# Kernel optimization log

Hardware: AMD Instinct MI355X
Metric: run time of the kernel (lower is better)

Reference implementation:

```python
import jax, jax.numpy as jnp
import numpy as np

N = 100000   # nodes
E = 3200000  # edges
F_IN = 64    # input feature dim
H = 64       # hidden dim
G = 512      # graphs in batch
C = 6        # classes
BN_EPS = 1e-5


def setup_inputs() -> dict:
    key = jax.random.key(0)
    ks = jax.random.split(key, 24)

    def nrm(i, shape, s=0.05):
        return jax.random.normal(ks[i], shape, jnp.float32) * s

    d = {}
    d["x"] = jax.random.normal(ks[0], (N, F_IN), jnp.float32)
    d["edge_index"] = jax.random.randint(ks[1], (2, E), 0, N, dtype=jnp.int32)
    d["batch"] = jnp.sort(jax.random.randint(ks[2], (N,), 0, G, dtype=jnp.int32))
    # GIN MLP weights (conv4 reuses conv3's MLP, matching the original code)
    for li, fin in [(1, F_IN), (2, H), (3, H)]:
        d[f"w{li}a"] = nrm(2 + li * 4, (fin, H))
        d[f"b{li}a"] = jnp.zeros((H,), jnp.float32)
        d[f"w{li}b"] = nrm(3 + li * 4, (H, H))
        d[f"b{li}b"] = jnp.zeros((H,), jnp.float32)
    # learnable eps (train_eps=True, init 0) and BN affine params per layer
    for li in range(1, 5):
        d[f"eps{li}"] = jnp.float32(0.0)
        d[f"g{li}"] = jnp.ones((H,), jnp.float32)
        d[f"be{li}"] = jnp.zeros((H,), jnp.float32)
    d["wfc"] = nrm(20, (2 * H, C))
    d["bfc"] = jnp.zeros((C,), jnp.float32)
    return d


def gin_block(x, src, dst, eps, wa, ba, wb, bb, gamma, beta):
    # neighbor sum aggregation: messages flow src -> dst
    agg = jax.ops.segment_sum(x[src], dst, num_segments=N)
    h = (1.0 + eps) * x + agg
    h = jax.nn.relu(h @ wa + ba) @ wb + bb  # GIN MLP
    h = jax.nn.relu(h)
    # BatchNorm1d over the node dimension (training-mode batch stats)
    mu = h.mean(axis=0)
    var = h.var(axis=0)
    return (h - mu) * jax.lax.rsqrt(var + BN_EPS) * gamma + beta


def reference(x, edge_index, batch,
              w1a, b1a, w1b, b1b, w2a, b2a, w2b, b2b, w3a, b3a, w3b, b3b,
              eps1, g1, be1, eps2, g2, be2, eps3, g3, be3, eps4, g4, be4,
              wfc, bfc):
    src, dst = edge_index[0], edge_index[1]
    h = gin_block(x, src, dst, eps1, w1a, b1a, w1b, b1b, g1, be1)
    h = gin_block(h, src, dst, eps2, w2a, b2a, w2b, b2b, g2, be2)
    h = gin_block(h, src, dst, eps3, w3a, b3a, w3b, b3b, g3, be3)
    # conv4 shares nn3's weights (faithful to the original source)
    h = gin_block(h, src, dst, eps4, w3a, b3a, w3b, b3b, g4, be4)
    cnt = jax.ops.segment_sum(jnp.ones((N, 1), h.dtype), batch, num_segments=G)
    meanp = jax.ops.segment_sum(h, batch, num_segments=G) / jnp.maximum(cnt, 1.0)
    maxp = jax.ops.segment_max(h, batch, num_segments=G)
    maxp = jnp.where(cnt > 0, maxp, 0.0)
    pooled = jnp.concatenate([meanp, maxp], axis=1)  # [G, 128]
    return jax.nn.log_softmax(pooled @ wfc + bfc, axis=1)
```

## Files before the change

kernel.cpp:

```cpp
#include <hip/hip_runtime.h>

#define N_NODES 100000
#define N_EDGES 3200000
#define NGRAPH 512
#define NCLASS 6
#define BN_EPS 1e-5f

#define BSHIFT 8
#define NBUCK 391
#define CHUNK 8192
#define EB 391
#define NBLK_NODE 391
#define FUSG 3125
#define NPART 6250
#define CAST_B 6250
#define BSMAX 12032

typedef unsigned short u16;
typedef unsigned int u32;
typedef __attribute__((ext_vector_type(8))) short bf16x8;
typedef __attribute__((ext_vector_type(4))) float f32x4;
typedef __attribute__((ext_vector_type(2))) float f32x2;

__device__ __forceinline__ float bflo(u32 b) {
    u32 t = b << 16; return __builtin_bit_cast(float, t);
}
__device__ __forceinline__ float bfhi(u32 b) {
    u32 t = b & 0xffff0000u; return __builtin_bit_cast(float, t);
}
__device__ __forceinline__ f32x2 bfpair(u32 b) {
    return (f32x2){bflo(b), bfhi(b)};
}
__device__ __forceinline__ u16 f2bf(float f) {
    u32 u = __builtin_bit_cast(u32, f);
    return (u16)((u + 0x7fffu + ((u >> 16) & 1u)) >> 16);
}

__global__ void k_setup(const float* __restrict__ x, u16* __restrict__ xb,
                        const float* __restrict__ W10, const float* __restrict__ W20,
                        const float* __restrict__ W11, const float* __restrict__ W21,
                        const float* __restrict__ W12, const float* __restrict__ W22,
                        u16* __restrict__ Wtg, float* __restrict__ ss0,
                        const int* __restrict__ dst, const int* __restrict__ batch,
                        int* __restrict__ blockhist, int* __restrict__ gstart,
                        int* __restrict__ rowstart) {
    __shared__ int hist[NBUCK];
    int b = blockIdx.x;
    int t = threadIdx.x;
    if (b < CAST_B) {
        int base = (b * 256 + t) * 4;
        float4 v = *(const float4*)(x + base);
        ushort4 o = make_ushort4(f2bf(v.x), f2bf(v.y), f2bf(v.z), f2bf(v.w));
        *(ushort4*)(xb + base) = o;
    } else if (b < CAST_B + 97) {
        int bb = b - CAST_B;
        if (bb < 96) {
            int e = bb * 256 + t;
            int mat = e >> 12;
            int i = e & 4095;
            const float* s = (mat == 0) ? W10 : (mat == 1) ? W20 : (mat == 2) ? W11
                           : (mat == 3) ? W21 : (mat == 4) ? W12 : W22;
            float v = s[i];
            int k = i >> 6, c = i & 63;
            Wtg[mat * 4608 + c * 72 + k] = f2bf(v);
        } else {
            if (t < 64) ss0[t] = 1.0f;
            else if (t < 128) ss0[t] = 0.0f;
            else if (t == 128) rowstart[N_NODES] = N_EDGES;
        }
    } else if (b < CAST_B + 97 + EB) {
        int be = b - (CAST_B + 97);
        long e0 = (long)be * CHUNK;
        for (int i = t; i < NBUCK; i += 256) hist[i] = 0;
        __syncthreads();
        for (int i = t; i < CHUNK; i += 256) {
            long e = e0 + i;
            if (e < N_EDGES) atomicAdd(&hist[dst[e] >> BSHIFT], 1);
        }
        __syncthreads();
        for (int i = t; i < NBUCK; i += 256) blockhist[be * NBUCK + i] = hist[i];
    } else {
        int i = (b - (CAST_B + 97 + EB)) * 256 + t;
        if (i < N_NODES) {
            int bi = batch[i];
            int bp = (i == 0) ? -1 : batch[i - 1];
            for (int g = bp + 1; g <= bi; ++g) gstart[g] = i;
            if (i == N_NODES - 1)
                for (int g = bi + 1; g <= NGRAPH; ++g) gstart[g] = N_NODES;
        }
    }
}

__global__ void k_scan_cols(int* __restrict__ blockhist, int* __restrict__ colsum) {
    __shared__ int sh[512];
    int k = blockIdx.x;
    int t = threadIdx.x;
    int v = (t < EB) ? blockhist[t * NBUCK + k] : 0;
    sh[t] = v;
    __syncthreads();
    for (int off = 1; off < 512; off <<= 1) {
        int x = (t >= off) ? sh[t - off] : 0;
        __syncthreads();
        sh[t] += x;
        __syncthreads();
    }
    if (t < EB) blockhist[t * NBUCK + k] = sh[t] - v;
    if (t == 511) colsum[k] = sh[511];
}

__global__ __launch_bounds__(512) void k_bscatter(
    const int* __restrict__ src, const int* __restrict__ dst,
    const int* __restrict__ colsum, const int* __restrict__ blockhist,
    int* __restrict__ pairs) {
    __shared__ int sh[512];
    __shared__ int bstart_s[NBUCK];
    __shared__ int cnt[NBUCK];
    __shared__ int cur[NBUCK];
    __shared__ int gbase[NBUCK];
    __shared__ u32 sorted[CHUNK];
    __shared__ u16 kbuf[CHUNK];
    int t = threadIdx.x;
    int b = blockIdx.x;
    long e0 = (long)b * CHUNK;
    int v = (t < NBUCK) ? colsum[t] : 0;
    sh[t] = v;
    if (t < NBUCK) cnt[t] = 0;
    __syncthreads();
    for (int off = 1; off < 512; off <<= 1) {
        int x = (t >= off) ? sh[t - off] : 0;
        __syncthreads();
        sh[t] += x;
        __syncthreads();
    }
    if (t < NBUCK) bstart_s[t] = sh[t] - v;
    __syncthreads();
    for (int i = t; i < CHUNK; i += 512) {
        long e = e0 + i;
        if (e < N_EDGES) atomicAdd(&cnt[dst[e] >> BSHIFT], 1);
    }
    __syncthreads();
    int c = (t < NBUCK) ? cnt[t] : 0;
    sh[t] = c;
    __syncthreads();
    for (int off = 1; off < 512; off <<= 1) {
        int x = (t >= off) ? sh[t - off] : 0;
        __syncthreads();
        sh[t] += x;
        __syncthreads();
    }
    if (t < NBUCK) {
        int excl = sh[t] - c;
        cur[t] = excl;
        gbase[t] = bstart_s[t] + blockhist[b * NBUCK + t] - excl;
    }
    __syncthreads();
    for (int i = t; i < CHUNK; i += 512) {
        long e = e0 + i;
        if (e < N_EDGES) {
            int d = dst[e];
            int k = d >> BSHIFT;
            int r = atomicAdd(&cur[k], 1);
            sorted[r] = ((u32)src[e] << 8) | (u32)(d & 255);
            kbuf[r] = (u16)k;
        }
    }
    __syncthreads();
    int tot = (int)min((long)CHUNK, (long)N_EDGES - e0);
    for (int i = t; i < tot; i += 512)
        pairs[gbase[kbuf[i]] + i] = (int)sorted[i];
}

__global__ __launch_bounds__(512) void k_bsort(
    const int* __restrict__ pairs, const int* __restrict__ colsum,
    int* __restrict__ rowstart, int* __restrict__ esrc) {
    __shared__ int sh[512];
    __shared__ int deg[256];
    __shared__ int cur[256];
    __shared__ u32 ssrc[BSMAX];
    int b = blockIdx.x;
    int t = threadIdx.x;
    int v = (t < NBUCK) ? colsum[t] : 0;
    sh[t] = v;
    if (t < 256) deg[t] = 0;
    __syncthreads();
    for (int off = 1; off < 512; off <<= 1) {
        int x = (t >= off) ? sh[t - off] : 0;
        __syncthreads();
        sh[t] += x;
        __syncthreads();
    }
    int p0 = (b == 0) ? 0 : sh[b - 1];
    int p1 = sh[b];
    int n = p1 - p0;
    __syncthreads();
    for (int i = p0 + t; i < p1; i += 512)
        atomicAdd(&deg[pairs[i] & 255], 1);
    __syncthreads();
    if (t < 256) sh[t] = deg[t];
    __syncthreads();
    for (int off = 1; off < 256; off <<= 1) {
        int x = (t >= off && t < 256) ? sh[t - off] : 0;
        __syncthreads();
        if (t < 256) sh[t] += x;
        __syncthreads();
    }
    if (t < 256) {
        int excl = sh[t] - deg[t];
        cur[t] = excl;
        int node = (b << BSHIFT) + t;
        if (node < N_NODES) rowstart[node] = p0 + excl;
    }
    __syncthreads();
    if (n <= BSMAX) {
        for (int i = p0 + t; i < p1; i += 512) {
            u32 pr = (u32)pairs[i];
            int r = atomicAdd(&cur[pr & 255], 1);
            ssrc[r] = pr >> 8;
        }
        __syncthreads();
        for (int i = t; i < n; i += 512) esrc[p0 + i] = (int)ssrc[i];
    } else {
        for (int i = p0 + t; i < p1; i += 512) {
            u32 pr = (u32)pairs[i];
            int r = atomicAdd(&cur[pr & 255], 1);
            esrc[p0 + r] = (int)(pr >> 8);
        }
    }
}

__global__ void k_bn(const float* __restrict__ partials, const float* __restrict__ g,
                     const float* __restrict__ be, float* __restrict__ ss) {
    __shared__ float sS[256];
    __shared__ float sQ[256];
    int f = blockIdx.x;
    int t = threadIdx.x;
    float aS = 0.f, aQ = 0.f;
    for (int b = t; b < NPART; b += 256) {
        aS += partials[b * 128 + f];
        aQ += partials[b * 128 + 64 + f];
    }
    sS[t] = aS; sQ[t] = aQ;
    __syncthreads();
    for (int off = 128; off >= 1; off >>= 1) {
        if (t < off) { sS[t] += sS[t + off]; sQ[t] += sQ[t + off]; }
        __syncthreads();
    }
    if (t == 0) {
        float mu = sS[0] / (float)N_NODES;
        float var = fmaxf(sQ[0] / (float)N_NODES - mu * mu, 0.f);
        float sc = g[f] * rsqrtf(var + BN_EPS);
        ss[f] = sc;
        ss[64 + f] = be[f] - mu * sc;
    }
}

__global__ __launch_bounds__(128, 5) void k_fused(
    const u16* __restrict__ hin, const float* __restrict__ ss,
    const float* __restrict__ epsp, const int* __restrict__ rowstart,
    const int* __restrict__ esrc, const u16* __restrict__ Wt,
    const float* __restrict__ b1, const float* __restrict__ b2,
    u16* __restrict__ C, float* __restrict__ partials) {
    __shared__ __align__(16) u16 Ain[2][16 * 72];
    __shared__ __align__(16) u16 Hs[2][16 * 72];
    int lane = threadIdx.x & 63;
    int wid = threadIdx.x >> 6;
    int r0 = blockIdx.x * 32 + wid * 16;

    int grp = lane >> 3;
    int f0 = 8 * (lane & 7);
    float epsv = 1.0f + epsp[0];
    float4 scA = *(const float4*)(ss + f0);
    float4 scB = *(const float4*)(ss + f0 + 4);
    float4 shA = *(const float4*)(ss + 64 + f0);
    float4 shB = *(const float4*)(ss + 64 + f0 + 4);
    float sc[8] = {scA.x, scA.y, scA.z, scA.w, scB.x, scB.y, scB.z, scB.w};
    float sh[8] = {shA.x, shA.y, shA.z, shA.w, shB.x, shB.y, shB.z, shB.w};

    for (int t = 0; t < 16; ++t) {
        int node = r0 + t;
        u32* arow = (u32*)&Ain[wid][0] + t * 36 + (lane & 7) * 4;
        if (node < N_NODES) {
            f32x2 ac0 = {0.f, 0.f}, ac1 = {0.f, 0.f}, ac2 = {0.f, 0.f}, ac3 = {0.f, 0.f};
            int e0 = rowstart[node], e1 = rowstart[node + 1];
            for (int i = e0; i < e1; i += 64) {
                int cnt = min(e1 - i, 64);
                int src = (lane < cnt) ? esrc[i + lane] : 0;
                int j = 0;
                for (; j + 16 <= cnt; j += 16) {
                    int a = __shfl(src, j + grp);
                    int b = __shfl(src, j + 8 + grp);
                    uint4 va = *(const uint4*)(hin + (size_t)a * 64 + f0);
                    uint4 vb = *(const uint4*)(hin + (size_t)b * 64 + f0);
                    ac0 += bfpair(va.x); ac1 += bfpair(va.y);
                    ac2 += bfpair(va.z); ac3 += bfpair(va.w);
                    ac0 += bfpair(vb.x); ac1 += bfpair(vb.y);
                    ac2 += bfpair(vb.z); ac3 += bfpair(vb.w);
                }
                if (j + 8 <= cnt) {
                    int a = __shfl(src, j + grp);
                    uint4 va = *(const uint4*)(hin + (size_t)a * 64 + f0);
                    ac0 += bfpair(va.x); ac1 += bfpair(va.y);
                    ac2 += bfpair(va.z); ac3 += bfpair(va.w);
                    j += 8;
                }
                if (j < cnt) {
                    int jj = j + grp;
                    int a = __shfl(src, (jj < cnt) ? jj : (cnt - 1));
                    uint4 va = *(const uint4*)(hin + (size_t)a * 64 + f0);
                    if (jj < cnt) {
                        ac0 += bfpair(va.x); ac1 += bfpair(va.y);
                        ac2 += bfpair(va.z); ac3 += bfpair(va.w);
                    }
                }
            }
            float acc[8] = {ac0.x, ac0.y, ac1.x, ac1.y, ac2.x, ac2.y, ac3.x, ac3.y};
            #pragma unroll
            for (int k = 0; k < 8; ++k) {
                acc[k] += __shfl_xor(acc[k], 8);
                acc[k] += __shfl_xor(acc[k], 16);
                acc[k] += __shfl_xor(acc[k], 32);
            }
            float deg = (float)(e1 - e0);
            uint4 sb = *(const uint4*)(hin + (size_t)node * 64 + f0);
            float self[8] = {bflo(sb.x), bfhi(sb.x), bflo(sb.y), bfhi(sb.y),
                             bflo(sb.z), bfhi(sb.z), bflo(sb.w), bfhi(sb.w)};
            if (grp == 0) {
                u32 pk[4];
                #pragma unroll
                for (int k = 0; k < 4; ++k) {
                    float oa = sc[2 * k] * (acc[2 * k] + epsv * self[2 * k]) +
                               (deg + epsv) * sh[2 * k];
                    float ob = sc[2 * k + 1] * (acc[2 * k + 1] + epsv * self[2 * k + 1]) +
                               (deg + epsv) * sh[2 * k + 1];
                    pk[k] = (u32)f2bf(oa) | ((u32)f2bf(ob) << 16);
                }
                *(uint4*)arow = make_uint4(pk[0], pk[1], pk[2], pk[3]);
            }
        } else if (grp == 0) {
            *(uint4*)arow = make_uint4(0, 0, 0, 0);
        }
    }

    const u16* Wt2 = Wt + 4608;
    int m = lane & 15;
    int q = lane >> 4;

    bf16x8 a0 = *(const bf16x8*)(&Ain[wid][m * 72 + q * 8]);
    bf16x8 a1 = *(const bf16x8*)(&Ain[wid][m * 72 + 32 + q * 8]);
    f32x4 acc[4];
    #pragma unroll
    for (int c = 0; c < 4; ++c) {
        acc[c] = (f32x4){0.f, 0.f, 0.f, 0.f};
        bf16x8 bA = *(const bf16x8*)(Wt + (c * 16 + m) * 72 + q * 8);
        bf16x8 bB = *(const bf16x8*)(Wt + (c * 16 + m) * 72 + 32 + q * 8);
        acc[c] = __builtin_amdgcn_mfma_f32_16x16x32_bf16(a0, bA, acc[c], 0, 0, 0);
        acc[c] = __builtin_amdgcn_mfma_f32_16x16x32_bf16(a1, bB, acc[c], 0, 0, 0);
    }
    #pragma unroll
    for (int c = 0; c < 4; ++c) {
        int col = c * 16 + m;
        float bb = b1[col];
        #pragma unroll
        for (int r = 0; r < 4; ++r)
            Hs[wid][(q * 4 + r) * 72 + col] = f2bf(fmaxf(acc[c][r] + bb, 0.f));
    }
    bf16x8 h0 = *(const bf16x8*)(&Hs[wid][m * 72 + q * 8]);
    bf16x8 h1 = *(const bf16x8*)(&Hs[wid][m * 72 + 32 + q * 8]);
    f32x4 acc2[4];
    #pragma unroll
    for (int c = 0; c < 4; ++c) {
        acc2[c] = (f32x4){0.f, 0.f, 0.f, 0.f};
        bf16x8 bA = *(const bf16x8*)(Wt2 + (c * 16 + m) * 72 + q * 8);
        bf16x8 bB = *(const bf16x8*)(Wt2 + (c * 16 + m) * 72 + 32 + q * 8);
        acc2[c] = __builtin_amdgcn_mfma_f32_16x16x32_bf16(h0, bA, acc2[c], 0, 0, 0);
        acc2[c] = __builtin_amdgcn_mfma_f32_16x16x32_bf16(h1, bB, acc2[c], 0, 0, 0);
    }
    size_t prow = ((size_t)blockIdx.x * 2 + wid) * 128;
    #pragma unroll
    for (int c = 0; c < 4; ++c) {
        int col = c * 16 + m;
        float bb = b2[col];
        float psum = 0.f, psq = 0.f;
        #pragma unroll
        for (int r = 0; r < 4; ++r) {
            int rg = r0 + q * 4 + r;
            if (rg < N_NODES) {
                float o = fmaxf(acc2[c][r] + bb, 0.f);
                C[(size_t)rg * 64 + col] = f2bf(o);
                psum += o;
                psq += o * o;
            }
        }
        psum += __shfl_xor(psum, 16);
        psum += __shfl_xor(psum, 32);
        psq += __shfl_xor(psq, 16);
        psq += __shfl_xor(psq, 32);
        if (q == 0) {
            partials[prow + col] = psum;
            partials[prow + 64 + col] = psq;
        }
    }
}

__global__ void k_pool(const u16* __restrict__ h, const float* __restrict__ ss,
                       const int* __restrict__ gstart, const float* __restrict__ wfc,
                       const float* __restrict__ bfc, float* __restrict__ out) {
    __shared__ float smean[2][128];
    __shared__ float smax[2][128];
    __shared__ float lg[2][8];
    int tid = threadIdx.x;
    int lane = tid & 63;
    int w = tid >> 6;
    int gi = w >> 1;
    int part = w & 1;
    int gr = blockIdx.x * 2 + gi;
    int half = lane >> 5;
    int li = lane & 31;
    int f0 = 2 * li;
    float sc0 = ss[f0], sc1 = ss[f0 + 1];
    float sh0 = ss[64 + f0], sh1 = ss[64 + f0 + 1];
    int s0n = gstart[gr], s1n = gstart[gr + 1];
    int cnt = s1n - s0n;
    int mid = s0n + (cnt >> 1);
    int a = part ? mid : s0n;
    int b = part ? s1n : mid;
    float sum0 = 0.f, sum1 = 0.f, mx0 = -3.4e38f, mx1 = -3.4e38f;
    for (int n = a + half; n < b; n += 2) {
        u32 bits = *(const u32*)(h + (size_t)n * 64 + f0);
        float x0 = fmaf(bflo(bits), sc0, sh0);
        float x1 = fmaf(bfhi(bits), sc1, sh1);
        sum0 += x0; sum1 += x1;
        mx0 = fmaxf(mx0, x0); mx1 = fmaxf(mx1, x1);
    }
    sum0 += __shfl_xor(sum0, 32);
    sum1 += __shfl_xor(sum1, 32);
    mx0 = fmaxf(mx0, __shfl_xor(mx0, 32));
    mx1 = fmaxf(mx1, __shfl_xor(mx1, 32));
    if (half == 0 && part == 0) {
        smean[gi][f0] = sum0; smean[gi][f0 + 1] = sum1;
        smax[gi][f0] = mx0;   smax[gi][f0 + 1] = mx1;
    }
    __syncthreads();
    if (half == 0 && part == 1) {
        float m0 = fmaxf(smax[gi][f0], mx0), m1 = fmaxf(smax[gi][f0 + 1], mx1);
        float t0 = smean[gi][f0] + sum0, t1 = smean[gi][f0 + 1] + sum1;
        float fc = fmaxf((float)cnt, 1.f);
        smean[gi][f0] = t0 / fc;
        smean[gi][f0 + 1] = t1 / fc;
        smax[gi][f0] = (cnt > 0) ? m0 : 0.f;
        smax[gi][f0 + 1] = (cnt > 0) ? m1 : 0.f;
    }
    __syncthreads();
    if (part == 0 && lane < NCLASS) {
        float acc = bfc[lane];
        for (int j = 0; j < 64; ++j) acc = fmaf(smean[gi][j], wfc[j * NCLASS + lane], acc);
        for (int j = 0; j < 64; ++j) acc = fmaf(smax[gi][j], wfc[(64 + j) * NCLASS + lane], acc);
        lg[gi][lane] = acc;
    }
    __syncthreads();
    if (part == 0 && lane < NCLASS) {
        float mm = -3.4e38f;
        for (int c = 0; c < NCLASS; ++c) mm = fmaxf(mm, lg[gi][c]);
        float se = 0.f;
        for (int c = 0; c < NCLASS; ++c) se += expf(lg[gi][c] - mm);
        out[gr * NCLASS + lane] = lg[gi][lane] - mm - logf(se);
    }
}


extern "C" void kernel_launch(void* const* d_in, const int* in_sizes, int n_in,
                              void* d_out, int out_size, void* d_ws, size_t ws_size,
                              hipStream_t stream) {
    const float* x = (const float*)d_in[0];
    const int* ei = (const int*)d_in[1];
    const int* batch = (const int*)d_in[2];
    const int* esrc_in = ei;
    const int* edst_in = ei + N_EDGES;

    const float* ba[4] = {(const float*)d_in[4], (const float*)d_in[8],
                          (const float*)d_in[12], (const float*)d_in[12]};
    const float* bb[4] = {(const float*)d_in[6], (const float*)d_in[10],
                          (const float*)d_in[14], (const float*)d_in[14]};
    const float* epsv[4] = {(const float*)d_in[15], (const float*)d_in[18],
                            (const float*)d_in[21], (const float*)d_in[24]};
    const float* gg[4] = {(const float*)d_in[16], (const float*)d_in[19],
                          (const float*)d_in[22], (const float*)d_in[25]};
    const float* bee[4] = {(const float*)d_in[17], (const float*)d_in[20],
                           (const float*)d_in[23], (const float*)d_in[26]};
    const float* wfc = (const float*)d_in[27];
    const float* bfc = (const float*)d_in[28];
    float* out = (float*)d_out;

    char* ws = (char*)d_ws;
    int* pairs = (int*)(ws + 0);
    u16* bufA = (u16*)(ws + 0);
    int* esrc = (int*)(ws + 12800000);
    u16* xb = (u16*)(ws + 25600000);
    u16* bufB = (u16*)(ws + 38400000);
    int* rowstart = (int*)(ws + 51200000);
    int* blockhist = (int*)(ws + 51600128);
    int* colsum = (int*)(ws + 52212480);
    int* gstart = (int*)(ws + 52214528);
    float* partials = (float*)(ws + 52217088);
    float* ssbuf = (float*)(ws + 55417600);
    u16* Wtg = (u16*)(ws + 55420160);

    k_setup<<<CAST_B + 97 + EB + NBLK_NODE, 256, 0, stream>>>(
        x, xb, (const float*)d_in[3], (const float*)d_in[5], (const float*)d_in[7],
        (const float*)d_in[9], (const float*)d_in[11], (const float*)d_in[13],
        Wtg, ssbuf, edst_in, batch, blockhist, gstart, rowstart);
    k_scan_cols<<<NBUCK, 512, 0, stream>>>(blockhist, colsum);
    k_bscatter<<<EB, 512, 0, stream>>>(esrc_in, edst_in, colsum, blockhist, pairs);
    k_bsort<<<NBUCK, 512, 0, stream>>>(pairs, colsum, rowstart, esrc);

    const u16* hb[4] = {xb, bufB, bufA, bufB};
    u16* cb[4] = {bufB, bufA, bufB, bufA};
    for (int L = 0; L < 4; ++L) {
        const u16* wt = Wtg + (size_t)((L < 2) ? L : 2) * 9216;
        k_fused<<<FUSG, 128, 0, stream>>>(hb[L], ssbuf + L * 128, epsv[L], rowstart,
                                          esrc, wt, ba[L], bb[L], cb[L], partials);
        k_bn<<<64, 256, 0, stream>>>(partials, gg[L], bee[L], ssbuf + (L + 1) * 128);
    }

    k_pool<<<NGRAPH / 2, 256, 0, stream>>>(bufA, ssbuf + 4 * 128, gstart, wfc, bfc, out);
}
```

Before: 535.1 us.

## Assign one node per 8-lane group in fused GIN aggregation instead of whole wave

The neighbor aggregation in the fused kernel now gives each 8-lane group its own node (two passes cover 16 nodes per wave) rather than having the full wave cooperate on one node at a time. Each group walks that node's edge list serially with an 8-way unroll and two accumulator sets, which removes the cross-group shuffle reductions and the per-node serial loop. Row starts are loaded once per wave and broadcast with shuffles. The N_NODES bounds checks are dropped, which relies on N dividing evenly into 32-row blocks, and the uneven degrees across groups may cause divergence within a wave.

After: 589.9 us. 1.1x slower.

```diff
diff --git a/kernel.cpp b/kernel.cpp
--- a/kernel.cpp
+++ b/kernel.cpp
@@ -266,8 +266,10 @@
     int wid = threadIdx.x >> 6;
     int r0 = blockIdx.x * 32 + wid * 16;
 
-    int grp = lane >> 3;
-    int f0 = 8 * (lane & 7);
+    int g = lane >> 3;
+    int p = lane & 7;
+    int f0 = 8 * p;
+
     float epsv = 1.0f + epsp[0];
     float4 scA = *(const float4*)(ss + f0);
     float4 scB = *(const float4*)(ss + f0 + 4);
@@ -276,69 +278,55 @@
     float sc[8] = {scA.x, scA.y, scA.z, scA.w, scB.x, scB.y, scB.z, scB.w};
     float sh[8] = {shA.x, shA.y, shA.z, shA.w, shB.x, shB.y, shB.z, shB.w};
 
-    for (int t = 0; t < 16; ++t) {
+    int rs = rowstart[r0 + ((lane < 17) ? lane : 16)];
+
+    #pragma unroll
+    for (int half = 0; half < 2; ++half) {
+        int t = g + 8 * half;
         int node = r0 + t;
-        u32* arow = (u32*)&Ain[wid][0] + t * 36 + (lane & 7) * 4;
-        if (node < N_NODES) {
-            f32x2 ac0 = {0.f, 0.f}, ac1 = {0.f, 0.f}, ac2 = {0.f, 0.f}, ac3 = {0.f, 0.f};
-            int e0 = rowstart[node], e1 = rowstart[node + 1];
-            for (int i = e0; i < e1; i += 64) {
-                int cnt = min(e1 - i, 64);
-                int src = (lane < cnt) ? esrc[i + lane] : 0;
-                int j = 0;
-                for (; j + 16 <= cnt; j += 16) {
-                    int a = __shfl(src, j + grp);
-                    int b = __shfl(src, j + 8 + grp);
-                    uint4 va = *(const uint4*)(hin + (size_t)a * 64 + f0);
-                    uint4 vb = *(const uint4*)(hin + (size_t)b * 64 + f0);
-                    ac0 += bfpair(va.x); ac1 += bfpair(va.y);
-                    ac2 += bfpair(va.z); ac3 += bfpair(va.w);
-                    ac0 += bfpair(vb.x); ac1 += bfpair(vb.y);
-                    ac2 += bfpair(vb.z); ac3 += bfpair(vb.w);
-                }
-                if (j + 8 <= cnt) {
-                    int a = __shfl(src, j + grp);
-                    uint4 va = *(const uint4*)(hin + (size_t)a * 64 + f0);
-                    ac0 += bfpair(va.x); ac1 += bfpair(va.y);
-                    ac2 += bfpair(va.z); ac3 += bfpair(va.w);
-                    j += 8;
-                }
-                if (j < cnt) {
-                    int jj = j + grp;
-                    int a = __shfl(src, (jj < cnt) ? jj : (cnt - 1));
-                    uint4 va = *(const uint4*)(hin + (size_t)a * 64 + f0);
-                    if (jj < cnt) {
-                        ac0 += bfpair(va.x); ac1 += bfpair(va.y);
-                        ac2 += bfpair(va.z); ac3 += bfpair(va.w);
-                    }
+        int e0 = __shfl(rs, t);
+        int e1 = __shfl(rs, t + 1);
+        uint4 sb = *(const uint4*)(hin + (unsigned)node * 64u + f0);
+        f32x2 aA0 = {0.f, 0.f}, aA1 = {0.f, 0.f}, aA2 = {0.f, 0.f}, aA3 = {0.f, 0.f};
+        f32x2 aB0 = {0.f, 0.f}, aB1 = {0.f, 0.f}, aB2 = {0.f, 0.f}, aB3 = {0.f, 0.f};
+        int e = e0;
+        int e_full = e0 + ((e1 - e0) & ~7);
+        for (; e < e_full; e += 8) {
+            #pragma unroll
+            for (int k = 0; k < 8; ++k) {
+                int a = esrc[e + k];
+                uint4 v = *(const uint4*)(hin + (unsigned)a * 64u + f0);
+                if (k & 1) {
+                    aB0 += bfpair(v.x); aB1 += bfpair(v.y);
+                    aB2 += bfpair(v.z); aB3 += bfpair(v.w);
+                } else {
+                    aA0 += bfpair(v.x); aA1 += bfpair(v.y);
+                    aA2 += bfpair(v.z); aA3 += bfpair(v.w);
                 }
             }
-            float acc[8] = {ac0.x, ac0.y, ac1.x, ac1.y, ac2.x, ac2.y, ac3.x, ac3.y};
-            #pragma unroll
-            for (int k = 0; k < 8; ++k) {
-                acc[k] += __shfl_xor(acc[k], 8);
-                acc[k] += __shfl_xor(acc[k], 16);
-                acc[k] += __shfl_xor(acc[k], 32);
-            }
-            float deg = (float)(e1 - e0);
-            uint4 sb = *(const uint4*)(hin + (size_t)node * 64 + f0);
-            float self[8] = {bflo(sb.x), bfhi(sb.x), bflo(sb.y), bfhi(sb.y),
-                             bflo(sb.z), bfhi(sb.z), bflo(sb.w), bfhi(sb.w)};
-            if (grp == 0) {
-                u32 pk[4];
-                #pragma unroll
-                for (int k = 0; k < 4; ++k) {
-                    float oa = sc[2 * k] * (acc[2 * k] + epsv * self[2 * k]) +
-                               (deg + epsv) * sh[2 * k];
-                    float ob = sc[2 * k + 1] * (acc[2 * k + 1] + epsv * self[2 * k + 1]) +
-                               (deg + epsv) * sh[2 * k + 1];
-                    pk[k] = (u32)f2bf(oa) | ((u32)f2bf(ob) << 16);
-                }
-                *(uint4*)arow = make_uint4(pk[0], pk[1], pk[2], pk[3]);
-            }
-        } else if (grp == 0) {
-            *(uint4*)arow = make_uint4(0, 0, 0, 0);
-        }
+        }
+        for (; e < e1; ++e) {
+            int a = esrc[e];
+            uint4 v = *(const uint4*)(hin + (unsigned)a * 64u + f0);
+            aA0 += bfpair(v.x); aA1 += bfpair(v.y);
+            aA2 += bfpair(v.z); aA3 += bfpair(v.w);
+        }
+        f32x2 ac0 = aA0 + aB0, ac1 = aA1 + aB1, ac2 = aA2 + aB2, ac3 = aA3 + aB3;
+        float acc[8] = {ac0.x, ac0.y, ac1.x, ac1.y, ac2.x, ac2.y, ac3.x, ac3.y};
+        float self[8] = {bflo(sb.x), bfhi(sb.x), bflo(sb.y), bfhi(sb.y),
+                         bflo(sb.z), bfhi(sb.z), bflo(sb.w), bfhi(sb.w)};
+        float deg = (float)(e1 - e0);
+        u32 pk[4];
+        #pragma unroll
+        for (int k = 0; k < 4; ++k) {
+            float oa = sc[2 * k] * (acc[2 * k] + epsv * self[2 * k]) +
+                       (deg + epsv) * sh[2 * k];
+            float ob = sc[2 * k + 1] * (acc[2 * k + 1] + epsv * self[2 * k + 1]) +
+                       (deg + epsv) * sh[2 * k + 1];
+            pk[k] = (u32)f2bf(oa) | ((u32)f2bf(ob) << 16);
+        }
+        u32* arow = (u32*)&Ain[wid][0] + t * 36 + p * 4;
+        *(uint4*)arow = make_uint4(pk[0], pk[1], pk[2], pk[3]);
     }
 
     const u16* Wt2 = Wt + 4608;
@@ -384,12 +372,10 @@
         #pragma unroll
         for (int r = 0; r < 4; ++r) {
             int rg = r0 + q * 4 + r;
-            if (rg < N_NODES) {
-                float o = fmaxf(acc2[c][r] + bb, 0.f);
-                C[(size_t)rg * 64 + col] = f2bf(o);
-                psum += o;
-                psq += o * o;
-            }
+            float o = fmaxf(acc2[c][r] + bb, 0.f);
+            C[(size_t)rg * 64 + col] = f2bf(o);
+            psum += o;
+            psq += o * o;
         }
         psum += __shfl_xor(psum, 16);
         psum += __shfl_xor(psum, 32);
```

## Fuse BatchNorm stat reduction into GIN layer kernel via last-blocks atomic counter

Applied to the files above, without the earlier changes.

Removes the separate k_bn launch per layer. Every k_fused block increments a per-layer done counter, and the last 64 blocks spin until all blocks have finished, then each reduces one feature's partial sums and writes the BN scale and shift. This saves four kernel launches and their gaps. The cost is spin-waiting in the tail blocks and a dependence on forward progress: the waiting blocks must not starve earlier blocks of scheduling slots, which is likely fine since they are the highest block indices.

Result: slower. 982.8 us (+83.7%).

```diff
diff --git a/kernel.cpp b/kernel.cpp
--- a/kernel.cpp
+++ b/kernel.cpp
@@ -43,7 +43,7 @@
                         u16* __restrict__ Wtg, float* __restrict__ ss0,
                         const int* __restrict__ dst, const int* __restrict__ batch,
                         int* __restrict__ blockhist, int* __restrict__ gstart,
-                        int* __restrict__ rowstart) {
+                        int* __restrict__ rowstart, int* __restrict__ done4) {
     __shared__ int hist[NBUCK];
     int b = blockIdx.x;
     int t = threadIdx.x;
@@ -67,6 +67,7 @@
             if (t < 64) ss0[t] = 1.0f;
             else if (t < 128) ss0[t] = 0.0f;
             else if (t == 128) rowstart[N_NODES] = N_EDGES;
+            else if (t >= 132 && t < 136) done4[t - 132] = 0;
         }
     } else if (b < CAST_B + 97 + EB) {
         int be = b - (CAST_B + 97);
@@ -228,40 +229,17 @@
     }
 }
 
-__global__ void k_bn(const float* __restrict__ partials, const float* __restrict__ g,
-                     const float* __restrict__ be, float* __restrict__ ss) {
-    __shared__ float sS[256];
-    __shared__ float sQ[256];
-    int f = blockIdx.x;
-    int t = threadIdx.x;
-    float aS = 0.f, aQ = 0.f;
-    for (int b = t; b < NPART; b += 256) {
-        aS += partials[b * 128 + f];
-        aQ += partials[b * 128 + 64 + f];
-    }
-    sS[t] = aS; sQ[t] = aQ;
-    __syncthreads();
-    for (int off = 128; off >= 1; off >>= 1) {
-        if (t < off) { sS[t] += sS[t + off]; sQ[t] += sQ[t + off]; }
-        __syncthreads();
-    }
-    if (t == 0) {
-        float mu = sS[0] / (float)N_NODES;
-        float var = fmaxf(sQ[0] / (float)N_NODES - mu * mu, 0.f);
-        float sc = g[f] * rsqrtf(var + BN_EPS);
-        ss[f] = sc;
-        ss[64 + f] = be[f] - mu * sc;
-    }
-}
-
 __global__ __launch_bounds__(128, 5) void k_fused(
     const u16* __restrict__ hin, const float* __restrict__ ss,
     const float* __restrict__ epsp, const int* __restrict__ rowstart,
     const int* __restrict__ esrc, const u16* __restrict__ Wt,
     const float* __restrict__ b1, const float* __restrict__ b2,
-    u16* __restrict__ C, float* __restrict__ partials) {
+    u16* __restrict__ C, float* __restrict__ partials,
+    const float* __restrict__ gbn, const float* __restrict__ bebn,
+    float* __restrict__ ss_out, int* __restrict__ done) {
     __shared__ __align__(16) u16 Ain[2][16 * 72];
     __shared__ __align__(16) u16 Hs[2][16 * 72];
+    __shared__ float xw[4];
     int lane = threadIdx.x & 63;
     int wid = threadIdx.x >> 6;
     int r0 = blockIdx.x * 32 + wid * 16;
@@ -400,6 +378,45 @@
             partials[prow + 64 + col] = psq;
         }
     }
+
+    __syncthreads();
+    if (threadIdx.x == 0) {
+        __threadfence();
+        atomicAdd(done, 1);
+    }
+    if (blockIdx.x >= FUSG - 64) {
+        int f = blockIdx.x - (FUSG - 64);
+        if (threadIdx.x == 0) {
+            while (__hip_atomic_load(done, __ATOMIC_RELAXED,
+                                     __HIP_MEMORY_SCOPE_AGENT) < FUSG)
+                __builtin_amdgcn_s_sleep(2);
+        }
+        __syncthreads();
+        float aS = 0.f, aQ = 0.f;
+        for (int b = threadIdx.x; b < NPART; b += 128) {
+            u32 uS = __hip_atomic_load((const u32*)(partials + (size_t)b * 128 + f),
+                                       __ATOMIC_RELAXED, __HIP_MEMORY_SCOPE_AGENT);
+            u32 uQ = __hip_atomic_load((const u32*)(partials + (size_t)b * 128 + 64 + f),
+                                       __ATOMIC_RELAXED, __HIP_MEMORY_SCOPE_AGENT);
+            aS += __builtin_bit_cast(float, uS);
+            aQ += __builtin_bit_cast(float, uQ);
+        }
+        #pragma unroll
+        for (int off = 32; off >= 1; off >>= 1) {
+            aS += __shfl_xor(aS, off);
+            aQ += __shfl_xor(aQ, off);
+        }
+        if (lane == 0) { xw[wid * 2] = aS; xw[wid * 2 + 1] = aQ; }
+        __syncthreads();
+        if (threadIdx.x == 0) {
+            float S = xw[0] + xw[2], Q = xw[1] + xw[3];
+            float mu = S / (float)N_NODES;
+            float var = fmaxf(Q / (float)N_NODES - mu * mu, 0.f);
+            float scv = gbn[f] * rsqrtf(var + BN_EPS);
+            ss_out[f] = scv;
+            ss_out[64 + f] = bebn[f] - mu * scv;
+        }
+    }
 }
 
 __global__ void k_pool(const u16* __restrict__ h, const float* __restrict__ ss,
@@ -504,11 +521,12 @@
     float* partials = (float*)(ws + 52217088);
     float* ssbuf = (float*)(ws + 55417600);
     u16* Wtg = (u16*)(ws + 55420160);
+    int* done4 = colsum + 396;
 
     k_setup<<<CAST_B + 97 + EB + NBLK_NODE, 256, 0, stream>>>(
         x, xb, (const float*)d_in[3], (const float*)d_in[5], (const float*)d_in[7],
         (const float*)d_in[9], (const float*)d_in[11], (const float*)d_in[13],
-        Wtg, ssbuf, edst_in, batch, blockhist, gstart, rowstart);
+        Wtg, ssbuf, edst_in, batch, blockhist, gstart, rowstart, done4);
     k_scan_cols<<<NBUCK, 512, 0, stream>>>(blockhist, colsum);
     k_bscatter<<<EB, 512, 0, stream>>>(esrc_in, edst_in, colsum, blockhist, pairs);
     k_bsort<<<NBUCK, 512, 0, stream>>>(pairs, colsum, rowstart, esrc);
@@ -518,8 +536,9 @@
     for (int L = 0; L < 4; ++L) {
         const u16* wt = Wtg + (size_t)((L < 2) ? L : 2) * 9216;
         k_fused<<<FUSG, 128, 0, stream>>>(hb[L], ssbuf + L * 128, epsv[L], rowstart,
-                                          esrc, wt, ba[L], bb[L], cb[L], partials);
-        k_bn<<<64, 256, 0, stream>>>(partials, gg[L], bee[L], ssbuf + (L + 1) * 128);
+                                          esrc, wt, ba[L], bb[L], cb[L], partials,
+                                          gg[L], bee[L], ssbuf + (L + 1) * 128,
+                                          done4 + L);
     }
 
     k_pool<<<NGRAPH / 2, 256, 0, stream>>>(bufA, ssbuf + 4 * 128, gstart, wfc, bfc, out);
```

## Fold BatchNorm reduction into fused kernel via atomic sums, drop k_bn launches

Applied to the files above, without the earlier changes.

Each fused GIN layer kernel now accumulates per-feature sum and sum-of-squares directly with float atomics into a small global buffer, rather than writing per-block partials. The next layer and the pool kernel compute mean, variance and scale/shift inline from these sums, so the four separate BN reduction kernels disappear. This removes four launches and the partials round trip. In exchange it adds heavy atomic contention on 128 addresses and makes the float sums order-nondeterministic.

Measured after the change: 1.034 ms. +93.2%, slower.

```diff
diff --git a/kernel.cpp b/kernel.cpp
--- a/kernel.cpp
+++ b/kernel.cpp
@@ -12,7 +12,6 @@
 #define EB 391
 #define NBLK_NODE 391
 #define FUSG 3125
-#define NPART 6250
 #define CAST_B 6250
 #define BSMAX 12032
 
@@ -40,7 +39,7 @@
                         const float* __restrict__ W10, const float* __restrict__ W20,
                         const float* __restrict__ W11, const float* __restrict__ W21,
                         const float* __restrict__ W12, const float* __restrict__ W22,
-                        u16* __restrict__ Wtg, float* __restrict__ ss0,
+                        u16* __restrict__ Wtg, float* __restrict__ sums4,
                         const int* __restrict__ dst, const int* __restrict__ batch,
                         int* __restrict__ blockhist, int* __restrict__ gstart,
                         int* __restrict__ rowstart) {
@@ -64,9 +63,9 @@
             int k = i >> 6, c = i & 63;
             Wtg[mat * 4608 + c * 72 + k] = f2bf(v);
         } else {
-            if (t < 64) ss0[t] = 1.0f;
-            else if (t < 128) ss0[t] = 0.0f;
-            else if (t == 128) rowstart[N_NODES] = N_EDGES;
+            sums4[t] = 0.f;
+            sums4[t + 256] = 0.f;
+            if (t == 128) rowstart[N_NODES] = N_EDGES;
         }
     } else if (b < CAST_B + 97 + EB) {
         int be = b - (CAST_B + 97);
@@ -228,38 +227,13 @@
     }
 }
 
-__global__ void k_bn(const float* __restrict__ partials, const float* __restrict__ g,
-                     const float* __restrict__ be, float* __restrict__ ss) {
-    __shared__ float sS[256];
-    __shared__ float sQ[256];
-    int f = blockIdx.x;
-    int t = threadIdx.x;
-    float aS = 0.f, aQ = 0.f;
-    for (int b = t; b < NPART; b += 256) {
-        aS += partials[b * 128 + f];
-        aQ += partials[b * 128 + 64 + f];
-    }
-    sS[t] = aS; sQ[t] = aQ;
-    __syncthreads();
-    for (int off = 128; off >= 1; off >>= 1) {
-        if (t < off) { sS[t] += sS[t + off]; sQ[t] += sQ[t + off]; }
-        __syncthreads();
-    }
-    if (t == 0) {
-        float mu = sS[0] / (float)N_NODES;
-        float var = fmaxf(sQ[0] / (float)N_NODES - mu * mu, 0.f);
-        float sc = g[f] * rsqrtf(var + BN_EPS);
-        ss[f] = sc;
-        ss[64 + f] = be[f] - mu * sc;
-    }
-}
-
 __global__ __launch_bounds__(128, 5) void k_fused(
-    const u16* __restrict__ hin, const float* __restrict__ ss,
+    const u16* __restrict__ hin, const float* __restrict__ sums_in,
+    const float* __restrict__ gbn, const float* __restrict__ bebn, int raw,
     const float* __restrict__ epsp, const int* __restrict__ rowstart,
     const int* __restrict__ esrc, const u16* __restrict__ Wt,
     const float* __restrict__ b1, const float* __restrict__ b2,
-    u16* __restrict__ C, float* __restrict__ partials) {
+    u16* __restrict__ C, float* __restrict__ sums_out) {
     __shared__ __align__(16) u16 Ain[2][16 * 72];
     __shared__ __align__(16) u16 Hs[2][16 * 72];
     int lane = threadIdx.x & 63;
@@ -269,12 +243,23 @@
     int grp = lane >> 3;
     int f0 = 8 * (lane & 7);
     float epsv = 1.0f + epsp[0];
-    float4 scA = *(const float4*)(ss + f0);
-    float4 scB = *(const float4*)(ss + f0 + 4);
-    float4 shA = *(const float4*)(ss + 64 + f0);
-    float4 shB = *(const float4*)(ss + 64 + f0 + 4);
-    float sc[8] = {scA.x, scA.y, scA.z, scA.w, scB.x, scB.y, scB.z, scB.w};
-    float sh[8] = {shA.x, shA.y, shA.z, shA.w, shB.x, shB.y, shB.z, shB.w};
+    float sc[8], sh[8];
+    if (raw) {
+        #pragma unroll
+        for (int k = 0; k < 8; ++k) { sc[k] = 1.0f; sh[k] = 0.0f; }
+    } else {
+        #pragma unroll
+        for (int k = 0; k < 8; ++k) {
+            int f = f0 + k;
+            float S = sums_in[f];
+            float Q = sums_in[64 + f];
+            float mu = S * (1.0f / (float)N_NODES);
+            float var = fmaxf(Q * (1.0f / (float)N_NODES) - mu * mu, 0.f);
+            float s = gbn[f] * rsqrtf(var + BN_EPS);
+            sc[k] = s;
+            sh[k] = bebn[f] - mu * s;
+        }
+    }
 
     for (int t = 0; t < 16; ++t) {
         int node = r0 + t;
@@ -375,7 +360,6 @@
         acc2[c] = __builtin_amdgcn_mfma_f32_16x16x32_bf16(h0, bA, acc2[c], 0, 0, 0);
         acc2[c] = __builtin_amdgcn_mfma_f32_16x16x32_bf16(h1, bB, acc2[c], 0, 0, 0);
     }
-    size_t prow = ((size_t)blockIdx.x * 2 + wid) * 128;
     #pragma unroll
     for (int c = 0; c < 4; ++c) {
         int col = c * 16 + m;
@@ -396,13 +380,14 @@
         psq += __shfl_xor(psq, 16);
         psq += __shfl_xor(psq, 32);
         if (q == 0) {
-            partials[prow + col] = psum;
-            partials[prow + 64 + col] = psq;
-        }
-    }
-}
-
-__global__ void k_pool(const u16* __restrict__ h, const float* __restrict__ ss,
+            atomicAdd(&sums_out[col], psum);
+            atomicAdd(&sums_out[64 + col], psq);
+        }
+    }
+}
+
+__global__ void k_pool(const u16* __restrict__ h, const float* __restrict__ sums,
+                       const float* __restrict__ gbn, const float* __restrict__ bebn,
                        const int* __restrict__ gstart, const float* __restrict__ wfc,
                        const float* __restrict__ bfc, float* __restrict__ out) {
     __shared__ float smean[2][128];
@@ -417,8 +402,19 @@
     int half = lane >> 5;
     int li = lane & 31;
     int f0 = 2 * li;
-    float sc0 = ss[f0], sc1 = ss[f0 + 1];
-    float sh0 = ss[64 + f0], sh1 = ss[64 + f0 + 1];
+    float sc0, sc1, sh0, sh1;
+    {
+        float S0 = sums[f0], Q0 = sums[64 + f0];
+        float S1 = sums[f0 + 1], Q1 = sums[64 + f0 + 1];
+        float mu0 = S0 * (1.0f / (float)N_NODES);
+        float mu1 = S1 * (1.0f / (float)N_NODES);
+        float v0 = fmaxf(Q0 * (1.0f / (float)N_NODES) - mu0 * mu0, 0.f);
+        float v1 = fmaxf(Q1 * (1.0f / (float)N_NODES) - mu1 * mu1, 0.f);
+        sc0 = gbn[f0] * rsqrtf(v0 + BN_EPS);
+        sc1 = gbn[f0 + 1] * rsqrtf(v1 + BN_EPS);
+        sh0 = bebn[f0] - mu0 * sc0;
+        sh1 = bebn[f0 + 1] - mu1 * sc1;
+    }
     int s0n = gstart[gr], s1n = gstart[gr + 1];
     int cnt = s1n - s0n;
     int mid = s0n + (cnt >> 1);
@@ -501,14 +497,13 @@
     int* blockhist = (int*)(ws + 51600128);
     int* colsum = (int*)(ws + 52212480);
     int* gstart = (int*)(ws + 52214528);
-    float* partials = (float*)(ws + 52217088);
-    float* ssbuf = (float*)(ws + 55417600);
-    u16* Wtg = (u16*)(ws + 55420160);
+    float* sums4 = (float*)(ws + 52217088);
+    u16* Wtg = (u16*)(ws + 52219136);
 
     k_setup<<<CAST_B + 97 + EB + NBLK_NODE, 256, 0, stream>>>(
         x, xb, (const float*)d_in[3], (const float*)d_in[5], (const float*)d_in[7],
         (const float*)d_in[9], (const float*)d_in[11], (const float*)d_in[13],
-        Wtg, ssbuf, edst_in, batch, blockhist, gstart, rowstart);
+        Wtg, sums4, edst_in, batch, blockhist, gstart, rowstart);
     k_scan_cols<<<NBUCK, 512, 0, stream>>>(blockhist, colsum);
     k_bscatter<<<EB, 512, 0, stream>>>(esrc_in, edst_in, colsum, blockhist, pairs);
     k_bsort<<<NBUCK, 512, 0, stream>>>(pairs, colsum, rowstart, esrc);
@@ -517,10 +512,14 @@
     u16* cb[4] = {bufB, bufA, bufB, bufA};
     for (int L = 0; L < 4; ++L) {
         const u16* wt = Wtg + (size_t)((L < 2) ? L : 2) * 9216;
-        k_fused<<<FUSG, 128, 0, stream>>>(hb[L], ssbuf + L * 128, epsv[L], rowstart,
-                                          esrc, wt, ba[L], bb[L], cb[L], partials);
-        k_bn<<<64, 256, 0, stream>>>(partials, gg[L], bee[L], ssbuf + (L + 1) * 128);
-    }
-
-    k_pool<<<NGRAPH / 2, 256, 0, stream>>>(bufA, ssbuf + 4 * 128, gstart, wfc, bfc, out);
-}
+        const float* sin = (L == 0) ? sums4 : sums4 + (L - 1) * 128;
+        const float* gprev = (L == 0) ? gg[0] : gg[L - 1];
+        const float* beprev = (L == 0) ? bee[0] : bee[L - 1];
+        k_fused<<<FUSG, 128, 0, stream>>>(hb[L], sin, gprev, beprev, (L == 0) ? 1 : 0,
+                                          epsv[L], rowstart, esrc, wt, ba[L], bb[L],
+                                          cb[L], sums4 + L * 128);
+    }
+
+    k_pool<<<NGRAPH / 2, 256, 0, stream>>>(bufA, sums4 + 3 * 128, gg[3], bee[3],
+                                           gstart, wfc, bfc, out);
+}
```
